# Performance work log

Hardware: AMD Instinct MI355X
Metric: run time of the kernel (lower is better)

The kernel has to match this reference:

```python
import jax, jax.numpy as jnp
import numpy as np


def _bilinear_resample(imgs, dvfs):
    # imgs: (B,H,W,C), dvfs: (B,H,W,2) with channel 0 = x(width) offset, 1 = y(height) offset
    B, H, W, C = imgs.shape
    fx = jnp.arange(W, dtype=imgs.dtype)[None, None, :] + dvfs[..., 0]  # (B,H,W)
    fy = jnp.arange(H, dtype=imgs.dtype)[None, :, None] + dvfs[..., 1]  # (B,H,W)

    x0f = jnp.floor(fx)
    y0f = jnp.floor(fy)
    wx = fx - x0f  # fractional weights
    wy = fy - y0f
    x0 = x0f.astype(jnp.int32)
    y0 = y0f.astype(jnp.int32)
    x1 = x0 + 1
    y1 = y0 + 1

    def gather(iy, ix):
        # zero-padding semantics for out-of-bounds corners (tf resampler behavior)
        valid = (ix >= 0) & (ix < W) & (iy >= 0) & (iy < H)
        ixc = jnp.clip(ix, 0, W - 1)
        iyc = jnp.clip(iy, 0, H - 1)
        vals = jax.vmap(lambda im, yy, xx: im[yy, xx])(imgs, iyc, ixc)  # (B,H,W,C)
        return vals * valid[..., None].astype(imgs.dtype)

    v00 = gather(y0, x0)
    v01 = gather(y0, x1)
    v10 = gather(y1, x0)
    v11 = gather(y1, x1)

    wx = wx[..., None]
    wy = wy[..., None]
    return (v00 * (1 - wx) * (1 - wy)
            + v01 * wx * (1 - wy)
            + v10 * (1 - wx) * wy
            + v11 * wx * wy)


def setup_inputs() -> dict:
    key = jax.random.key(0)
    k1, k2 = jax.random.split(key)
    B, H, W = 32, 1024, 1024
    imgs = jax.random.normal(k1, (B, H, W, 1), dtype=jnp.float32)
    dvfs = jax.random.normal(k2, (B, H, W, 2), dtype=jnp.float32)
    return {"imgs": imgs, "dvfs": dvfs}


def reference(imgs, dvfs):
    return _bilinear_resample(imgs, dvfs)
```

## Files before the change

### kernel.cpp

```cpp
#include <hip/hip_runtime.h>


#define H_DIM 1024
#define W_DIM 1024
#define HW_SHIFT 20
#define TILE 64
#define HALO 8
#define S_DIM (TILE + 2 * HALO + 1)

__device__ __forceinline__ float gather_zp(const float* __restrict__ img,
                                           int yy, int xx) {
    bool valid = (xx >= 0) & (xx < W_DIM) & (yy >= 0) & (yy < H_DIM);
    int xc = min(max(xx, 0), W_DIM - 1);
    int yc = min(max(yy, 0), H_DIM - 1);
    float v = img[yc * W_DIM + xc];
    return valid ? v : 0.0f;
}

__global__ __launch_bounds__(256) void bilerp_kernel(
        const float* __restrict__ imgs,
        const float* __restrict__ dvfs,
        float* __restrict__ out) {
    __shared__ float tile[S_DIM * S_DIM];

    const int gx0 = blockIdx.x * TILE;
    const int gy0 = blockIdx.y * TILE;
    const int b   = blockIdx.z;
    const int tid = threadIdx.x;

    const float* __restrict__ img = imgs + ((long long)b << HW_SHIFT);

    const int x_base = gx0 - HALO;
    const int y_base = gy0 - HALO;
    for (int idx = tid; idx < S_DIM * S_DIM; idx += 256) {
        int r = idx / S_DIM;
        int c = idx - r * S_DIM;
        int gy = y_base + r;
        int gx = x_base + c;
        float v = 0.0f;
        if ((unsigned)gy < (unsigned)H_DIM && (unsigned)gx < (unsigned)W_DIM)
            v = img[(gy << 10) + gx];
        tile[idx] = v;
    }
    __syncthreads();

    const int tx = tid & 63;
    const int ty = tid >> 6;
    const float* __restrict__ dv_img =
        dvfs + (((long long)b << HW_SHIFT) << 1);
    float* __restrict__ out_img = out + ((long long)b << HW_SHIFT);

    for (int i = 0; i < 16; ++i) {
        int y = gy0 + (i << 2) + ty;
        int x = gx0 + tx;
        int pix = (y << 10) + x;

        union { double d64; float2 f2; } cvt;
        cvt.d64 = __builtin_nontemporal_load(
            reinterpret_cast<const double*>(dv_img) + pix);
        float dx = cvt.f2.x;
        float dy = cvt.f2.y;

        float fx = (float)x + dx;
        float fy = (float)y + dy;
        float x0f = floorf(fx);
        float y0f = floorf(fy);
        float wx = fx - x0f;
        float wy = fy - y0f;
        int x0 = (int)x0f;
        int y0 = (int)y0f;

        int lx = x0 - x_base;
        int ly = y0 - y_base;

        float v00, v01, v10, v11;
        if ((unsigned)lx < (unsigned)(S_DIM - 1) &&
            (unsigned)ly < (unsigned)(S_DIM - 1)) {
            const float* p = &tile[ly * S_DIM + lx];
            v00 = p[0];
            v01 = p[1];
            v10 = p[S_DIM];
            v11 = p[S_DIM + 1];
        } else {
            v00 = gather_zp(img, y0,     x0);
            v01 = gather_zp(img, y0,     x0 + 1);
            v10 = gather_zp(img, y0 + 1, x0);
            v11 = gather_zp(img, y0 + 1, x0 + 1);
        }

        float res = v00 * (1.0f - wx) * (1.0f - wy)
                  + v01 * wx          * (1.0f - wy)
                  + v10 * (1.0f - wx) * wy
                  + v11 * wx          * wy;

        __builtin_nontemporal_store(res, out_img + pix);
    }
}

extern "C" void kernel_launch(void* const* d_in, const int* in_sizes, int n_in,
                              void* d_out, int out_size, void* d_ws, size_t ws_size,
                              hipStream_t stream) {
    const float* imgs = (const float*)d_in[0];
    const float* dvfs = (const float*)d_in[1];
    float* out = (float*)d_out;

    dim3 grid(W_DIM / TILE, H_DIM / TILE, 32);
    bilerp_kernel<<<grid, 256, 0, stream>>>(imgs, dvfs, out);
}
```

Baseline: 527.7 us.

## Prefetch displacement fields before tile load, vectorize tile fill, use lerp FMAs

```diff
diff --git a/kernel.cpp b/kernel.cpp
--- a/kernel.cpp
+++ b/kernel.cpp
@@ -6,7 +6,9 @@
 #define HW_SHIFT 20
 #define TILE 64
 #define HALO 8
-#define S_DIM (TILE + 2 * HALO + 1)
+#define S_W 80
+#define S_H 80
+#define S_W4 20
 
 __device__ __forceinline__ float gather_zp(const float* __restrict__ img,
                                            int yy, int xx) {
@@ -21,66 +23,67 @@
         const float* __restrict__ imgs,
         const float* __restrict__ dvfs,
         float* __restrict__ out) {
-    __shared__ float tile[S_DIM * S_DIM];
+    __shared__ float tile[S_H * S_W];
 
     const int gx0 = blockIdx.x * TILE;
     const int gy0 = blockIdx.y * TILE;
     const int b   = blockIdx.z;
     const int tid = threadIdx.x;
+    const int tx  = tid & 63;
+    const int ty  = tid >> 6;
 
-    const float* __restrict__ img = imgs + ((long long)b << HW_SHIFT);
+    const float*  __restrict__ img    = imgs + ((long long)b << HW_SHIFT);
+    const double* __restrict__ dv_img =
+        reinterpret_cast<const double*>(dvfs) + ((long long)b << HW_SHIFT);
+    float* __restrict__ out_img = out + ((long long)b << HW_SHIFT);
+
+    const int x = gx0 + tx;
+
+    float2 d[16];
+    #pragma unroll
+    for (int i = 0; i < 16; ++i) {
+        int y = gy0 + (i << 2) + ty;
+        union { double u; float2 f; } cvt;
+        cvt.u = __builtin_nontemporal_load(dv_img + ((y << 10) + x));
+        d[i] = cvt.f;
+    }
 
     const int x_base = gx0 - HALO;
     const int y_base = gy0 - HALO;
-    for (int idx = tid; idx < S_DIM * S_DIM; idx += 256) {
-        int r = idx / S_DIM;
-        int c = idx - r * S_DIM;
+    for (int q = tid; q < S_H * S_W4; q += 256) {
+        int r = q / S_W4;
+        int c = q - r * S_W4;
         int gy = y_base + r;
-        int gx = x_base + c;
-        float v = 0.0f;
+        int gx = x_base + (c << 2);
+        float4 v = make_float4(0.f, 0.f, 0.f, 0.f);
         if ((unsigned)gy < (unsigned)H_DIM && (unsigned)gx < (unsigned)W_DIM)
-            v = img[(gy << 10) + gx];
-        tile[idx] = v;
+            v = *reinterpret_cast<const float4*>(img + (gy << 10) + gx);
+        *reinterpret_cast<float4*>(&tile[r * S_W + (c << 2)]) = v;
     }
     __syncthreads();
 
-    const int tx = tid & 63;
-    const int ty = tid >> 6;
-    const float* __restrict__ dv_img =
-        dvfs + (((long long)b << HW_SHIFT) << 1);
-    float* __restrict__ out_img = out + ((long long)b << HW_SHIFT);
-
+    #pragma unroll
     for (int i = 0; i < 16; ++i) {
         int y = gy0 + (i << 2) + ty;
-        int x = gx0 + tx;
-        int pix = (y << 10) + x;
-
-        union { double d64; float2 f2; } cvt;
-        cvt.d64 = __builtin_nontemporal_load(
-            reinterpret_cast<const double*>(dv_img) + pix);
-        float dx = cvt.f2.x;
-        float dy = cvt.f2.y;
-
-        float fx = (float)x + dx;
-        float fy = (float)y + dy;
+        float fx = (float)x + d[i].x;
+        float fy = (float)y + d[i].y;
         float x0f = floorf(fx);
         float y0f = floorf(fy);
         float wx = fx - x0f;
         float wy = fy - y0f;
         int x0 = (int)x0f;
         int y0 = (int)y0f;
-
         int lx = x0 - x_base;
         int ly = y0 - y_base;
 
         float v00, v01, v10, v11;
-        if ((unsigned)lx < (unsigned)(S_DIM - 1) &&
-            (unsigned)ly < (unsigned)(S_DIM - 1)) {
-            const float* p = &tile[ly * S_DIM + lx];
+        if ((unsigned)lx < (unsigned)(S_W - 1) &&
+            (unsigned)ly < (unsigned)(S_H - 1)) {
+            const float* p = &tile[ly * S_W + lx];
             v00 = p[0];
             v01 = p[1];
-            v10 = p[S_DIM];
-            v11 = p[S_DIM + 1];
+            v10 = p[S_W];
+            v11 = p[S_W + 1];
         } else {
             v00 = gather_zp(img, y0,     x0);
             v01 = gather_zp(img, y0,     x0 + 1);
@@ -88,12 +91,11 @@
             v11 = gather_zp(img, y0 + 1, x0 + 1);
         }
 
-        float res = v00 * (1.0f - wx) * (1.0f - wy)
-                  + v01 * wx          * (1.0f - wy)
-                  + v10 * (1.0f - wx) * wy
-                  + v11 * wx          * wy;
+        float top = fmaf(wx, v01 - v00, v00);
+        float bot = fmaf(wx, v11 - v10, v10);
+        float res = fmaf(wy, bot - top, top);
 
-        __builtin_nontemporal_store(res, out_img + pix);
+        __builtin_nontemporal_store(res, out_img + ((y << 10) + x));
     }
 }
 
```

Result: no change. 522.4 us (-1.0%).
